# Performance work log

Measured on AMD Instinct MI355X. Metric: run time of the kernel, lower is better.

Reference implementation:

```python
import jax, jax.numpy as jnp
import numpy as np

B, N, F_IN, F_OUT = 8, 2048, 128, 128


def setup_inputs() -> dict:
    key = jax.random.key(0)
    k1, k2, k3, k4 = jax.random.split(key, 4)
    h = jax.random.normal(k1, (B, N, F_IN), dtype=jnp.float32)
    adj = (jax.random.uniform(k2, (B, N, N)) > 0.5).astype(jnp.float32)
    adj = jnp.maximum(adj, jnp.eye(N, dtype=jnp.float32)[None])
    # torch nn.Linear weights: W is [out_features, in_features], a is [1, 2*out_features]
    W = jax.random.normal(k3, (F_OUT, F_IN), dtype=jnp.float32) * 0.05
    a = jax.random.normal(k4, (1, 2 * F_OUT), dtype=jnp.float32) * 0.05
    return {"h": h, "adj": adj, "W": W, "a": a}


def reference(h, adj, W, a):
    # Wh = W(h): [B, N, F_OUT]
    Wh = jnp.einsum("bnf,of->bno", h, W)
    # attn_fc(concat(Wh_i, Wh_j)) == (Wh_i @ a1) + (Wh_j @ a2): exact split of the
    # linear layer, avoiding the O(B*N*N*2F) concat intermediate.
    a1 = a[0, :F_OUT]
    a2 = a[0, F_OUT:]
    e_i = Wh @ a1  # [B, N]  score contribution of destination node i
    e_j = Wh @ a2  # [B, N]  score contribution of source node j
    e = e_i[:, :, None] + e_j[:, None, :]  # [B, N, N]
    e = e + (1.0 - adj) * (-1e9)
    alpha = jax.nn.softmax(e, axis=-1)  # [B, N, N]
    # weighted aggregation: h_out[b,i] = sum_j alpha[b,i,j] * Wh[b,j]
    h_out = jnp.einsum("bij,bjo->bio", alpha, Wh)
    return h_out
```

## Files before the change

### kernel.cpp

```cpp
#include <hip/hip_runtime.h>
#include <stdint.h>

#define AS1 __attribute__((address_space(1)))
#define AS3 __attribute__((address_space(3)))

typedef __bf16 bf16x8 __attribute__((ext_vector_type(8)));
typedef float f32x4 __attribute__((ext_vector_type(4)));

constexpr int NB = 8;
constexpr int N  = 2048;
constexpr int F  = 128;

__device__ __forceinline__ void async16(const void* g, void* l) {
    __builtin_amdgcn_global_load_lds((const AS1 void*)g, (AS3 void*)l, 16, 0, 0);
}

__device__ __forceinline__ unsigned short bf16r(float f) {
    unsigned u = __float_as_uint(f);
    return (unsigned short)((u + 0x7FFFu + ((u >> 16) & 1u)) >> 16);
}

__global__ __launch_bounds__(256) void k1_wh(const float* __restrict__ h,
                                             const float* __restrict__ W,
                                             unsigned short* __restrict__ Wht) {
    const int tid  = threadIdx.x;
    const int lane = tid & 63, wid = tid >> 6;
    const int quad = lane >> 4, l15 = lane & 15;
    const int wm = wid >> 1, wn = wid & 1;
    const int m0 = blockIdx.x * 64;
    const int batch = m0 >> 11;
    const int nbase = m0 & 2047;

    f32x4 acc[2][4] = {};

#pragma unroll
    for (int kk = 0; kk < 4; ++kk) {
        const int k = kk * 32 + quad * 8;
        bf16x8 afr[2], bfr[4];
#pragma unroll
        for (int rt = 0; rt < 2; ++rt) {
            const float* src = h + (size_t)(m0 + wm * 32 + rt * 16 + l15) * F + k;
            float4 x0 = *(const float4*)src;
            float4 x1 = *(const float4*)(src + 4);
            afr[rt][0] = (__bf16)x0.x; afr[rt][1] = (__bf16)x0.y;
            afr[rt][2] = (__bf16)x0.z; afr[rt][3] = (__bf16)x0.w;
            afr[rt][4] = (__bf16)x1.x; afr[rt][5] = (__bf16)x1.y;
            afr[rt][6] = (__bf16)x1.z; afr[rt][7] = (__bf16)x1.w;
        }
#pragma unroll
        for (int ct = 0; ct < 4; ++ct) {
            const int o = wn * 64 + ct * 16 + l15;
            const float* src = W + (size_t)o * F + k;
            float4 x0 = *(const float4*)src;
            float4 x1 = *(const float4*)(src + 4);
            bfr[ct][0] = (__bf16)x0.x; bfr[ct][1] = (__bf16)x0.y;
            bfr[ct][2] = (__bf16)x0.z; bfr[ct][3] = (__bf16)x0.w;
            bfr[ct][4] = (__bf16)x1.x; bfr[ct][5] = (__bf16)x1.y;
            bfr[ct][6] = (__bf16)x1.z; bfr[ct][7] = (__bf16)x1.w;
        }
#pragma unroll
        for (int rt = 0; rt < 2; ++rt)
#pragma unroll
            for (int ct = 0; ct < 4; ++ct)
                acc[rt][ct] = __builtin_amdgcn_mfma_f32_16x16x32_bf16(
                    afr[rt], bfr[ct], acc[rt][ct], 0, 0, 0);
    }

#pragma unroll
    for (int rt = 0; rt < 2; ++rt)
#pragma unroll
        for (int ct = 0; ct < 4; ++ct) {
            const int o  = wn * 64 + ct * 16 + l15;
            const int nl = nbase + wm * 32 + rt * 16 + quad * 4;
            ushort4 v;
            v.x = bf16r(acc[rt][ct][0]); v.y = bf16r(acc[rt][ct][1]);
            v.z = bf16r(acc[rt][ct][2]); v.w = bf16r(acc[rt][ct][3]);
            *(ushort4*)&Wht[(size_t)batch * F * N + (size_t)o * N + nl] = v;
        }
}

__global__ __launch_bounds__(256) void k2_p(const unsigned short* __restrict__ Wht,
                                            const float* __restrict__ a,
                                            float* __restrict__ p) {
    const int gid = blockIdx.x * 256 + threadIdx.x;
    const int b = gid >> 10;
    const int n = (gid & 1023) * 2;
    const unsigned short* base = Wht + (size_t)b * F * N + n;
    float a0 = 0.f, a1 = 0.f;
#pragma unroll 8
    for (int o = 0; o < F; ++o) {
        unsigned v = *(const unsigned*)(base + (size_t)o * N);
        float f0 = __uint_as_float(v << 16);
        float f1 = __uint_as_float(v & 0xFFFF0000u);
        float w = a[F + o];
        a0 += f0 * w;
        a1 += f1 * w;
    }
    p[b * N + n]     = expf(a0);
    p[b * N + n + 1] = expf(a1);
}

__global__ __launch_bounds__(256, 2) void k3_attn(const float* __restrict__ adj,
                                                  const unsigned short* __restrict__ Wht,
                                                  const float* __restrict__ p,
                                                  float* __restrict__ out) {
    __shared__ __align__(16) float         At[2][32 * 64];
    __shared__ __align__(16) unsigned short Bt[2][128 * 64];
    __shared__ __align__(16) float         Pt[2][64];

    const int tid  = threadIdx.x;
    const int lane = tid & 63, wid = tid >> 6;
    const int quad = lane >> 4, l15 = lane & 15;
    const int wm = wid >> 1, wn = wid & 1;
    const int b  = blockIdx.x >> 6;
    const int i0 = (blockIdx.x & 63) * 32;

    const float* adjb          = adj + (size_t)b * N * N;
    const unsigned short* Bb   = Wht + (size_t)b * F * N;
    const float* pb            = p + b * N;

    auto stageA = [&](int buf, int j0) {
#pragma unroll
        for (int is = 0; is < 2; ++is) {
            int Fo  = wid * 1024 + is * 4096 + lane * 16;
            int row = Fo >> 8;
            int cg  = ((Fo >> 4) & 15) ^ (row & 15);
            const float* g = adjb + (size_t)(i0 + row) * N + j0 + cg * 4;
            async16(g, (char*)&At[buf][0] + wid * 1024 + is * 4096);
        }
    };
    auto stageB = [&](int buf, int j0) {
#pragma unroll
        for (int is = 0; is < 4; ++is) {
            int Fo = wid * 1024 + is * 4096 + lane * 16;
            int o  = Fo >> 7;
            int cg = ((Fo >> 4) & 7) ^ (o & 7);
            const unsigned short* g = Bb + (size_t)o * N + j0 + cg * 8;
            async16(g, (char*)&Bt[buf][0] + wid * 1024 + is * 4096);
        }
    };

    f32x4 acc[4] = {};
    f32x4 dacc = {};
    const bf16x8 ones = {(__bf16)1.0f, (__bf16)1.0f, (__bf16)1.0f, (__bf16)1.0f,
                         (__bf16)1.0f, (__bf16)1.0f, (__bf16)1.0f, (__bf16)1.0f};

    stageA(0, 0);
    stageB(0, 0);
    if (tid < 64) Pt[0][tid] = pb[tid];

    for (int ch = 0; ch < 32; ++ch) {
        const int cur = ch & 1, nxt = cur ^ 1;
        __syncthreads();
        if (ch + 1 < 32) {
            stageA(nxt, (ch + 1) * 64);
            stageB(nxt, (ch + 1) * 64);
            if (tid < 64) Pt[nxt][tid] = pb[(ch + 1) * 64 + tid];
        }
#pragma unroll
        for (int ss = 0; ss < 2; ++ss) {
            const float* pt = &Pt[cur][ss * 32 + quad * 8];
            float4 pp0 = *(const float4*)pt;
            float4 pp1 = *(const float4*)(pt + 4);

            const int r = wm * 16 + l15;
            const float* arow = &At[cur][r * 64];
            const int c0 = (ss * 8 + quad * 2)     ^ l15;
            const int c1 = (ss * 8 + quad * 2 + 1) ^ l15;
            float4 x0 = *(const float4*)(arow + c0 * 4);
            float4 x1 = *(const float4*)(arow + c1 * 4);

            bf16x8 af;
            af[0] = (__bf16)(x0.x * pp0.x); af[1] = (__bf16)(x0.y * pp0.y);
            af[2] = (__bf16)(x0.z * pp0.z); af[3] = (__bf16)(x0.w * pp0.w);
            af[4] = (__bf16)(x1.x * pp1.x); af[5] = (__bf16)(x1.y * pp1.y);
            af[6] = (__bf16)(x1.z * pp1.z); af[7] = (__bf16)(x1.w * pp1.w);

#pragma unroll
            for (int ct = 0; ct < 4; ++ct) {
                const int o  = wn * 64 + ct * 16 + l15;
                const int cb = (ss * 4 + quad) ^ (o & 7);
                bf16x8 bfv = *(const bf16x8*)((const char*)&Bt[cur][0] + o * 128 + cb * 16);
                acc[ct] = __builtin_amdgcn_mfma_f32_16x16x32_bf16(af, bfv, acc[ct], 0, 0, 0);
            }
            dacc = __builtin_amdgcn_mfma_f32_16x16x32_bf16(af, ones, dacc, 0, 0, 0);
        }
    }

    float inv[4];
#pragma unroll
    for (int g = 0; g < 4; ++g) inv[g] = 1.0f / dacc[g];

    float* ob = out + (size_t)b * N * F;
#pragma unroll
    for (int ct = 0; ct < 4; ++ct) {
        const int o = wn * 64 + ct * 16 + l15;
#pragma unroll
        for (int g = 0; g < 4; ++g) {
            const int i = i0 + wm * 16 + quad * 4 + g;
            ob[(size_t)i * F + o] = acc[ct][g] * inv[g];
        }
    }
}

extern "C" void kernel_launch(void* const* d_in, const int* in_sizes, int n_in,
                              void* d_out, int out_size, void* d_ws, size_t ws_size,
                              hipStream_t stream) {
    const float* h   = (const float*)d_in[0];
    const float* adj = (const float*)d_in[1];
    const float* W   = (const float*)d_in[2];
    const float* a   = (const float*)d_in[3];
    float* out = (float*)d_out;

    unsigned short* Wht = (unsigned short*)d_ws;
    float* p = (float*)((char*)d_ws + (size_t)4 * 1024 * 1024);

    k1_wh<<<NB * N / 64, 256, 0, stream>>>(h, W, Wht);
    k2_p<<<NB * N / (2 * 256), 256, 0, stream>>>(Wht, a, p);
    k3_attn<<<NB * (N / 32), 256, 0, stream>>>(adj, Wht, p, out);
}
```

Baseline: 229.4 us.

## Pre-scale Wh by exp weights into MFMA-fragment layout and drop LDS staging

Stores Wh in a blocked layout (8 rows by 128 features) that matches the MFMA B-fragment, and folds the exp(e_j) factor into a pre-scaled bf16 copy of Wh in the second kernel. The attention kernel then converts adj to bf16 without multiplying and loads B fragments and the exp vector straight from global memory, with no LDS double-buffering or barriers. The row-sum denominator now uses the exp vector as the MFMA B operand. This removes LDS traffic, the per-chunk __syncthreads and the per-element multiply, but relies on L2 and register prefetch for latency hiding and rounds exp weights to bf16.

```diff
diff --git a/kernel.cpp b/kernel.cpp
--- a/kernel.cpp
+++ b/kernel.cpp
@@ -1,8 +1,5 @@
 #include <hip/hip_runtime.h>
 #include <stdint.h>
-
-#define AS1 __attribute__((address_space(1)))
-#define AS3 __attribute__((address_space(3)))
 
 typedef __bf16 bf16x8 __attribute__((ext_vector_type(8)));
 typedef float f32x4 __attribute__((ext_vector_type(4)));
@@ -11,18 +8,18 @@
 constexpr int N  = 2048;
 constexpr int F  = 128;
 
-__device__ __forceinline__ void async16(const void* g, void* l) {
-    __builtin_amdgcn_global_load_lds((const AS1 void*)g, (AS3 void*)l, 16, 0, 0);
-}
-
 __device__ __forceinline__ unsigned short bf16r(float f) {
     unsigned u = __float_as_uint(f);
     return (unsigned short)((u + 0x7FFFu + ((u >> 16) & 1u)) >> 16);
 }
+__device__ __forceinline__ float bf2f(unsigned short s) {
+    return __uint_as_float(((unsigned)s) << 16);
+}
+
 
 __global__ __launch_bounds__(256) void k1_wh(const float* __restrict__ h,
                                              const float* __restrict__ W,
-                                             unsigned short* __restrict__ Wht) {
+                                             unsigned short* __restrict__ Wb) {
     const int tid  = threadIdx.x;
     const int lane = tid & 63, wid = tid >> 6;
     const int quad = lane >> 4, l15 = lane & 15;
@@ -71,43 +68,40 @@
 #pragma unroll
         for (int ct = 0; ct < 4; ++ct) {
             const int o  = wn * 64 + ct * 16 + l15;
-            const int nl = nbase + wm * 32 + rt * 16 + quad * 4;
+            const int n0 = nbase + wm * 32 + rt * 16 + quad * 4;
+            size_t off = (size_t)batch * N * F + (size_t)(n0 >> 3) * 1024 + o * 8 + (n0 & 7);
             ushort4 v;
             v.x = bf16r(acc[rt][ct][0]); v.y = bf16r(acc[rt][ct][1]);
             v.z = bf16r(acc[rt][ct][2]); v.w = bf16r(acc[rt][ct][3]);
-            *(ushort4*)&Wht[(size_t)batch * F * N + (size_t)o * N + nl] = v;
+            *(ushort4*)&Wb[off] = v;
         }
 }
 
-__global__ __launch_bounds__(256) void k2_p(const unsigned short* __restrict__ Wht,
-                                            const float* __restrict__ a,
-                                            float* __restrict__ p) {
+__global__ __launch_bounds__(256) void k2_scale(const unsigned short* __restrict__ Wb,
+                                               const float* __restrict__ a,
+                                               unsigned short* __restrict__ Wb2,
+                                               unsigned short* __restrict__ p16) {
     const int gid = blockIdx.x * 256 + threadIdx.x;
-    const int b = gid >> 10;
-    const int n = (gid & 1023) * 2;
-    const unsigned short* base = Wht + (size_t)b * F * N + n;
-    float a0 = 0.f, a1 = 0.f;
+    const int b = gid >> 11, j = gid & 2047;
+    const size_t base = (size_t)b * N * F + (size_t)(j >> 3) * 1024 + (j & 7);
+    const unsigned short* src = Wb + base;
+    float e = 0.f;
 #pragma unroll 8
-    for (int o = 0; o < F; ++o) {
-        unsigned v = *(const unsigned*)(base + (size_t)o * N);
-        float f0 = __uint_as_float(v << 16);
-        float f1 = __uint_as_float(v & 0xFFFF0000u);
-        float w = a[F + o];
-        a0 += f0 * w;
-        a1 += f1 * w;
-    }
-    p[b * N + n]     = expf(a0);
-    p[b * N + n + 1] = expf(a1);
+    for (int o = 0; o < F; ++o)
+        e += bf2f(src[o * 8]) * a[F + o];
+    unsigned short pb = bf16r(expf(e));
+    p16[gid] = pb;
+    const float pf = bf2f(pb);
+    unsigned short* dst = Wb2 + base;
+#pragma unroll 8
+    for (int o = 0; o < F; ++o)
+        dst[o * 8] = bf16r(pf * bf2f(src[o * 8]));
 }
 
 __global__ __launch_bounds__(256, 2) void k3_attn(const float* __restrict__ adj,
-                                                  const unsigned short* __restrict__ Wht,
-                                                  const float* __restrict__ p,
+                                                  const unsigned short* __restrict__ Wb2,
+                                                  const unsigned short* __restrict__ p16,
                                                   float* __restrict__ out) {
-    __shared__ __align__(16) float         At[2][32 * 64];
-    __shared__ __align__(16) unsigned short Bt[2][128 * 64];
-    __shared__ __align__(16) float         Pt[2][64];
-
     const int tid  = threadIdx.x;
     const int lane = tid & 63, wid = tid >> 6;
     const int quad = lane >> 4, l15 = lane & 15;
@@ -115,76 +109,34 @@
     const int b  = blockIdx.x >> 6;
     const int i0 = (blockIdx.x & 63) * 32;
 
-    const float* adjb          = adj + (size_t)b * N * N;
-    const unsigned short* Bb   = Wht + (size_t)b * F * N;
-    const float* pb            = p + b * N;
-
-    auto stageA = [&](int buf, int j0) {
-#pragma unroll
-        for (int is = 0; is < 2; ++is) {
-            int Fo  = wid * 1024 + is * 4096 + lane * 16;
-            int row = Fo >> 8;
-            int cg  = ((Fo >> 4) & 15) ^ (row & 15);
-            const float* g = adjb + (size_t)(i0 + row) * N + j0 + cg * 4;
-            async16(g, (char*)&At[buf][0] + wid * 1024 + is * 4096);
-        }
-    };
-    auto stageB = [&](int buf, int j0) {
-#pragma unroll
-        for (int is = 0; is < 4; ++is) {
-            int Fo = wid * 1024 + is * 4096 + lane * 16;
-            int o  = Fo >> 7;
-            int cg = ((Fo >> 4) & 7) ^ (o & 7);
-            const unsigned short* g = Bb + (size_t)o * N + j0 + cg * 8;
-            async16(g, (char*)&Bt[buf][0] + wid * 1024 + is * 4096);
-        }
-    };
+    const float* ar = adj + (size_t)b * N * N + (size_t)(i0 + wm * 16 + l15) * N + quad * 8;
+    const char* bB = (const char*)(Wb2 + (size_t)b * N * F) + quad * 2048 + wn * 1024 + l15 * 16;
+    const unsigned short* pq = p16 + b * N + quad * 8;
 
     f32x4 acc[4] = {};
     f32x4 dacc = {};
-    const bf16x8 ones = {(__bf16)1.0f, (__bf16)1.0f, (__bf16)1.0f, (__bf16)1.0f,
-                         (__bf16)1.0f, (__bf16)1.0f, (__bf16)1.0f, (__bf16)1.0f};
 
-    stageA(0, 0);
-    stageB(0, 0);
-    if (tid < 64) Pt[0][tid] = pb[tid];
+#pragma unroll 4
+    for (int kb = 0; kb < N; kb += 32) {
+        f32x4 x0 = __builtin_nontemporal_load((const f32x4*)(ar + kb));
+        f32x4 x1 = __builtin_nontemporal_load((const f32x4*)(ar + kb + 4));
+        bf16x8 bp = *(const bf16x8*)(pq + kb);
+        bf16x8 b0 = *(const bf16x8*)(bB + (size_t)kb * 256);
+        bf16x8 b1 = *(const bf16x8*)(bB + (size_t)kb * 256 + 256);
+        bf16x8 b2 = *(const bf16x8*)(bB + (size_t)kb * 256 + 512);
+        bf16x8 b3 = *(const bf16x8*)(bB + (size_t)kb * 256 + 768);
 
-    for (int ch = 0; ch < 32; ++ch) {
-        const int cur = ch & 1, nxt = cur ^ 1;
-        __syncthreads();
-        if (ch + 1 < 32) {
-            stageA(nxt, (ch + 1) * 64);
-            stageB(nxt, (ch + 1) * 64);
-            if (tid < 64) Pt[nxt][tid] = pb[(ch + 1) * 64 + tid];
-        }
-#pragma unroll
-        for (int ss = 0; ss < 2; ++ss) {
-            const float* pt = &Pt[cur][ss * 32 + quad * 8];
-            float4 pp0 = *(const float4*)pt;
-            float4 pp1 = *(const float4*)(pt + 4);
+        bf16x8 af;
+        af[0] = (__bf16)x0[0]; af[1] = (__bf16)x0[1];
+        af[2] = (__bf16)x0[2]; af[3] = (__bf16)x0[3];
+        af[4] = (__bf16)x1[0]; af[5] = (__bf16)x1[1];
+        af[6] = (__bf16)x1[2]; af[7] = (__bf16)x1[3];
 
-            const int r = wm * 16 + l15;
-            const float* arow = &At[cur][r * 64];
-            const int c0 = (ss * 8 + quad * 2)     ^ l15;
-            const int c1 = (ss * 8 + quad * 2 + 1) ^ l15;
-            float4 x0 = *(const float4*)(arow + c0 * 4);
-            float4 x1 = *(const float4*)(arow + c1 * 4);
-
-            bf16x8 af;
-            af[0] = (__bf16)(x0.x * pp0.x); af[1] = (__bf16)(x0.y * pp0.y);
-            af[2] = (__bf16)(x0.z * pp0.z); af[3] = (__bf16)(x0.w * pp0.w);
-            af[4] = (__bf16)(x1.x * pp1.x); af[5] = (__bf16)(x1.y * pp1.y);
-            af[6] = (__bf16)(x1.z * pp1.z); af[7] = (__bf16)(x1.w * pp1.w);
-
-#pragma unroll
-            for (int ct = 0; ct < 4; ++ct) {
-                const int o  = wn * 64 + ct * 16 + l15;
-                const int cb = (ss * 4 + quad) ^ (o & 7);
-                bf16x8 bfv = *(const bf16x8*)((const char*)&Bt[cur][0] + o * 128 + cb * 16);
-                acc[ct] = __builtin_amdgcn_mfma_f32_16x16x32_bf16(af, bfv, acc[ct], 0, 0, 0);
-            }
-            dacc = __builtin_amdgcn_mfma_f32_16x16x32_bf16(af, ones, dacc, 0, 0, 0);
-        }
+        acc[0] = __builtin_amdgcn_mfma_f32_16x16x32_bf16(af, b0, acc[0], 0, 0, 0);
+        acc[1] = __builtin_amdgcn_mfma_f32_16x16x32_bf16(af, b1, acc[1], 0, 0, 0);
+        acc[2] = __builtin_amdgcn_mfma_f32_16x16x32_bf16(af, b2, acc[2], 0, 0, 0);
+        acc[3] = __builtin_amdgcn_mfma_f32_16x16x32_bf16(af, b3, acc[3], 0, 0, 0);
+        dacc   = __builtin_amdgcn_mfma_f32_16x16x32_bf16(af, bp, dacc, 0, 0, 0);
     }
 
     float inv[4];
@@ -198,7 +150,7 @@
 #pragma unroll
         for (int g = 0; g < 4; ++g) {
             const int i = i0 + wm * 16 + quad * 4 + g;
-            ob[(size_t)i * F + o] = acc[ct][g] * inv[g];
+            __builtin_nontemporal_store(acc[ct][g] * inv[g], &ob[(size_t)i * F + o]);
         }
     }
 }
@@ -212,10 +164,11 @@
     const float* a   = (const float*)d_in[3];
     float* out = (float*)d_out;
 
-    unsigned short* Wht = (unsigned short*)d_ws;
-    float* p = (float*)((char*)d_ws + (size_t)4 * 1024 * 1024);
+    unsigned short* Wb  = (unsigned short*)d_ws;
+    unsigned short* Wb2 = (unsigned short*)((char*)d_ws + (4u << 20));
+    unsigned short* p16 = (unsigned short*)((char*)d_ws + (8u << 20));
 
-    k1_wh<<<NB * N / 64, 256, 0, stream>>>(h, W, Wht);
-    k2_p<<<NB * N / (2 * 256), 256, 0, stream>>>(Wht, a, p);
-    k3_attn<<<NB * (N / 32), 256, 0, stream>>>(adj, Wht, p, out);
+    k1_wh<<<NB * N / 64, 256, 0, stream>>>(h, W, Wb);
+    k2_scale<<<NB * N / 256, 256, 0, stream>>>(Wb, a, Wb2, p16);
+    k3_attn<<<NB * (N / 32), 256, 0, stream>>>(adj, Wb2, p16, out);
 }
```

Result: slower. 282.9 us (+23.3%).
